# Kernel tuning notes

Measured on AMD Instinct MI355X. Metric: run time of the kernel, lower is better.

Reference implementation:

```python
import jax, jax.numpy as jnp
import numpy as np

# Reconstructed GTS forecasting module (DCGRU encoder-decoder, eval mode / no teacher forcing).
N = 5000        # nodes_num
U = 32          # rnn_units
IN = 1          # node_features per step
K = 2           # max_diffusion_step -> supports [X, A@X, A@A@X]
T_ENC = 12
T_DEC = 12
DIN = (K + 1) * (IN + U)


def setup_inputs() -> dict:
    key = jax.random.key(0)
    ks = jax.random.split(key, 12)
    def p(k, shape, scale=0.1):
        return jax.random.normal(k, shape, dtype=jnp.float32) * scale
    inputs = jax.random.normal(ks[0], (N, T_ENC), dtype=jnp.float32)
    targets = jax.random.normal(ks[1], (N, T_DEC), dtype=jnp.float32)
    adj = jax.random.uniform(ks[2], (N, N), dtype=jnp.float32)
    adj = adj / jnp.sum(adj, axis=1, keepdims=True)  # random-walk normalized support
    return {
        'inputs': inputs, 'targets': targets, 'adj_matrix': adj,
        'enc_Wg': p(ks[3], (DIN, 2 * U)), 'enc_bg': jnp.zeros((2 * U,), jnp.float32),
        'enc_Wc': p(ks[4], (DIN, U)),     'enc_bc': jnp.zeros((U,), jnp.float32),
        'dec_Wg': p(ks[5], (DIN, 2 * U)), 'dec_bg': jnp.zeros((2 * U,), jnp.float32),
        'dec_Wc': p(ks[6], (DIN, U)),     'dec_bc': jnp.zeros((U,), jnp.float32),
        'dec_Wp': p(ks[7], (U, 1)),       'dec_bp': jnp.zeros((1,), jnp.float32),
    }


def _gconv(x, h, adj, W, b):
    # diffusion graph convolution over supports [I, A, A^2]
    xh = jnp.concatenate([x, h], axis=-1)          # [N, IN+U]
    x1 = adj @ xh                                  # [N, IN+U]
    x2 = adj @ x1                                  # [N, IN+U]
    return jnp.concatenate([xh, x1, x2], axis=-1) @ W + b


def _dcgru_step(x, h, adj, Wg, bg, Wc, bc):
    ru = jax.nn.sigmoid(_gconv(x, h, adj, Wg, bg))  # [N, 2U]
    r, u = jnp.split(ru, 2, axis=-1)
    c = jnp.tanh(_gconv(x, r * h, adj, Wc, bc))
    return u * h + (1.0 - u) * c


def reference(inputs, targets, adj_matrix, enc_Wg, enc_bg, enc_Wc, enc_bc,
              dec_Wg, dec_bg, dec_Wc, dec_bc, dec_Wp, dec_bp):
    # ---- encoder: scan DCGRU over encoder_length timesteps ----
    def enc_step(h, xt):  # xt: [N]
        h = _dcgru_step(xt[:, None], h, adj_matrix, enc_Wg, enc_bg, enc_Wc, enc_bc)
        return h, None
    h0 = jnp.zeros((N, U), inputs.dtype)
    h_enc, _ = jax.lax.scan(enc_step, h0, inputs.T)
    go = jnp.zeros((N, 1), inputs.dtype)
    def dec_step(carry, _):
        h, x = carry
        h = _dcgru_step(x, h, adj_matrix, dec_Wg, dec_bg, dec_Wc, dec_bc)
        out = h @ dec_Wp + dec_bp  # [N, 1]
        return (h, out), out
    _, outs = jax.lax.scan(dec_step, (h_enc, go), None, length=T_DEC)
    # torch.cat(outputs, dim=-1) -> [N, T_DEC]
    return outs[:, :, 0].T
```

## Files before the change

### kernel.cpp

```cpp
#include <hip/hip_runtime.h>
#include <type_traits>

constexpr int NN = 5000;
constexpr int NP = 5120;
constexpr int TT = 12;
constexpr int UU = 32;
constexpr int FP = 48;
constexpr int FR = 33;
constexpr int DN = 99;
constexpr int BN = 16;
constexpr int BNODE = 32;
constexpr int KC = 128;
constexpr int NKC = NP / KC;
constexpr int CPW = NKC / 8;
constexpr int GRID_MM = (NN + BNODE - 1) / BNODE;
constexpr int CHE = FP * KC;
constexpr int ACH = BN * KC;
constexpr int PB = FP * BNODE;

typedef __attribute__((ext_vector_type(8))) short short8;
typedef __attribute__((ext_vector_type(4))) float f32x4;

__device__ __forceinline__ unsigned short f2bf(float x) {
  union { float f; unsigned u; } c; c.f = x;
  return (unsigned short)((c.u + 0x7FFFu + ((c.u >> 16) & 1u)) >> 16);
}

__device__ __forceinline__ int flatXF(int f, int node) {
  int chunk = node >> 7;
  int ks = (node >> 5) & 3;
  int q = (node >> 3) & 3;
  int j = node & 7;
  int t3 = f >> 4;
  int m = f & 15;
  return chunk * CHE + t3 * 2048 + ks * 512 + (m + 16 * q) * 8 + j;
}

__global__ void k_zero(uint4* __restrict__ p, int n) {
  int i = blockIdx.x * 256 + threadIdx.x;
  if (i < n) p[i] = make_uint4(0u, 0u, 0u, 0u);
}

__global__ void k_cast2(const float* __restrict__ adj, unsigned short* __restrict__ adjb) {
  int gid = blockIdx.x * 256 + threadIdx.x;
  int tile = gid >> 8;
  int r2 = gid & 255;
  int nt = tile / NKC, c = tile - nt * NKC;
  int ks = r2 >> 6;
  int qm = r2 & 63;
  int q = qm >> 4, m = qm & 15;
  int n = nt * 16 + m;
  int k = c * 128 + ks * 32 + q * 8;
  union { short8 s; unsigned short u[8]; } o;
  if (n < NN && k < NN) {
    const f32x4* a = reinterpret_cast<const f32x4*>(adj + (size_t)n * NN + k);
    f32x4 x0 = __builtin_nontemporal_load(a);
    f32x4 x1 = __builtin_nontemporal_load(a + 1);
    o.u[0] = f2bf(x0.x); o.u[1] = f2bf(x0.y); o.u[2] = f2bf(x0.z); o.u[3] = f2bf(x0.w);
    o.u[4] = f2bf(x1.x); o.u[5] = f2bf(x1.y); o.u[6] = f2bf(x1.z); o.u[7] = f2bf(x1.w);
  } else {
    o.u[0] = 0; o.u[1] = 0; o.u[2] = 0; o.u[3] = 0;
    o.u[4] = 0; o.u[5] = 0; o.u[6] = 0; o.u[7] = 0;
  }
  *reinterpret_cast<short8*>(adjb + (size_t)gid * 8) = o.s;
}

__global__ void k_initx0(const float* __restrict__ in, float* __restrict__ xf,
                         unsigned short* __restrict__ xb) {
  int n = blockIdx.x * 256 + threadIdx.x;
  if (n >= NP) return;
  float v = (n < NN) ? in[(size_t)n * TT] : 0.f;
  xf[n] = v;
  xb[flatXF(0, n)] = f2bf(v);
}

template <int EPI, bool USEBF>
__global__ __launch_bounds__(512, 2) void k_gemm(
    const unsigned short* __restrict__ adjb, const float* __restrict__ adjf,
    const unsigned short* __restrict__ rhs,
    float* __restrict__ outF, unsigned short* __restrict__ outB,
    const float* __restrict__ s0F, const float* __restrict__ s1F,
    const float* __restrict__ W, const float* __restrict__ bias,
    float* __restrict__ hT, float* __restrict__ uT,
    float* __restrict__ xoF, unsigned short* __restrict__ xoB,
    const float* __restrict__ inp, const float* __restrict__ Wp,
    const float* __restrict__ bp, float* __restrict__ dout,
    int mode, int tnext, int dstep) {
  constexpr int WC = (EPI == 1) ? 64 : 32;
  __shared__ float smemF[PB * 8 + FP * 33];
  float* Pv = smemF;
  float* x2s = smemF + PB * 8;
  float* Ws = smemF;

  const int tid = threadIdx.x;
  const int wave = tid >> 6;
  const int lane = tid & 63;
  const int m = lane & 15;
  const int q = lane >> 4;
  const int nodeBase = blockIdx.x * BNODE;

  f32x4 acc[2][3] = {};
  short8 aCur[2][4], aNxt[2][4];

  auto loadA = [&](int i, short8 (&b)[2][4]) {
    if constexpr (USEBF) {
      const int ch = wave * CPW + i;
#pragma unroll
      for (int h = 0; h < 2; ++h) {
        const unsigned short* a0 =
            adjb + ((size_t)(2 * blockIdx.x + h) * NKC + ch) * ACH + lane * 8;
#pragma unroll
        for (int ks = 0; ks < 4; ++ks)
          b[h][ks] = *reinterpret_cast<const short8*>(a0 + ks * 512);
      }
    } else {
      const int k0 = (wave * CPW + i) * KC;
#pragma unroll
      for (int h = 0; h < 2; ++h) {
        int gnh = nodeBase + h * 16 + m;
        const float* a0 = adjf + (size_t)((gnh < NN) ? gnh : NN - 1) * NN;
#pragma unroll
        for (int ks = 0; ks < 4; ++ks) {
          int kb = k0 + ks * 32 + q * 8;
          union { short8 s; unsigned short u[8]; } p0;
          if (kb + 8 <= NN) {
            float4 x0 = *(const float4*)(a0 + kb);
            float4 x1 = *(const float4*)(a0 + kb + 4);
            p0.u[0] = f2bf(x0.x); p0.u[1] = f2bf(x0.y); p0.u[2] = f2bf(x0.z); p0.u[3] = f2bf(x0.w);
            p0.u[4] = f2bf(x1.x); p0.u[5] = f2bf(x1.y); p0.u[6] = f2bf(x1.z); p0.u[7] = f2bf(x1.w);
          } else {
            for (int j = 0; j < 8; ++j) {
              int k = kb + j;
              p0.u[j] = (k < NN) ? f2bf(a0[k]) : (unsigned short)0;
            }
          }
          b[h][ks] = p0.s;
        }
      }
    }
  };

  loadA(0, aCur);
#pragma unroll
  for (int i = 0; i < CPW; ++i) {
    const int ch = wave * CPW + i;
    short8 cx[12];
    const unsigned short* xb = rhs + (size_t)ch * CHE + lane * 8;
#pragma unroll
    for (int t3 = 0; t3 < 3; ++t3)
#pragma unroll
      for (int ks = 0; ks < 4; ++ks)
        cx[t3 * 4 + ks] = *(const short8*)(xb + t3 * 2048 + ks * 512);
    if (i + 1 < CPW) loadA(i + 1, aNxt);
#pragma unroll
    for (int ks = 0; ks < 4; ++ks) {
#pragma unroll
      for (int h = 0; h < 2; ++h) {
        acc[h][0] = __builtin_amdgcn_mfma_f32_16x16x32_bf16(cx[ks], aCur[h][ks], acc[h][0], 0, 0, 0);
        acc[h][1] = __builtin_amdgcn_mfma_f32_16x16x32_bf16(cx[4 + ks], aCur[h][ks], acc[h][1], 0, 0, 0);
        acc[h][2] = __builtin_amdgcn_mfma_f32_16x16x32_bf16(cx[8 + ks], aCur[h][ks], acc[h][2], 0, 0, 0);
      }
    }
#pragma unroll
    for (int h = 0; h < 2; ++h)
#pragma unroll
      for (int ks = 0; ks < 4; ++ks) aCur[h][ks] = aNxt[h][ks];
  }

#pragma unroll
  for (int h = 0; h < 2; ++h)
#pragma unroll
    for (int t3 = 0; t3 < 3; ++t3)
#pragma unroll
      for (int r = 0; r < 4; ++r)
        Pv[wave * PB + (t3 * 16 + q * 4 + r) * BNODE + h * 16 + m] = acc[h][t3][r];
  __syncthreads();

  if constexpr (EPI == 0) {
    for (int e = tid; e < PB; e += 512) {
      int f = e >> 5, n = e & 31;
      float v = 0.f;
#pragma unroll
      for (int w = 0; w < 8; ++w) v += Pv[w * PB + e];
      int gn2 = nodeBase + n;
      if (gn2 >= NN) v = 0.f;
      outF[(size_t)f * NP + gn2] = v;
      outB[flatXF(f, gn2)] = f2bf(v);
    }
  } else {
    for (int e = tid; e < PB; e += 512) {
      int f = e >> 5, n = e & 31;
      float v = 0.f;
#pragma unroll
      for (int w = 0; w < 8; ++w) v += Pv[w * PB + e];
      x2s[f * 33 + n] = v;
    }
    __syncthreads();
    for (int i = tid; i < DN * WC; i += 512) Ws[i] = W[i];
    __syncthreads();
    const int nl = tid & 15;
    const int cg = tid >> 4;
    float hwv[2];
#pragma unroll
    for (int nh = 0; nh < 2; ++nh) {
      const int nl2 = nh * 16 + nl;
      const int gn2 = nodeBase + nl2;
      const bool valid = gn2 < NN;
      const int gnc = valid ? gn2 : NN - 1;
      if constexpr (EPI == 1) {
        float a0 = bias[cg], a1 = bias[cg + 32];
        for (int f = 0; f < FR; ++f) {
          float fe = s0F[(size_t)f * NP + gnc];
          a0 += fe * Ws[f * WC + cg]; a1 += fe * Ws[f * WC + cg + 32];
        }
        for (int f = 0; f < FR; ++f) {
          float fe = s1F[(size_t)f * NP + gnc];
          a0 += fe * Ws[(FR + f) * WC + cg]; a1 += fe * Ws[(FR + f) * WC + cg + 32];
        }
        for (int f = 0; f < FR; ++f) {
          float fe = x2s[f * 33 + nl2];
          a0 += fe * Ws[(2 * FR + f) * WC + cg]; a1 += fe * Ws[(2 * FR + f) * WC + cg + 32];
        }
        float r = 1.f / (1.f + expf(-a0));
        float hv = hT[(size_t)cg * NP + gnc];
        float xc = valid ? r * hv : 0.f;
        xoF[(size_t)(1 + cg) * NP + gn2] = xc;
        xoB[flatXF(1 + cg, gn2)] = f2bf(xc);
        float u = 1.f / (1.f + expf(-a1));
        uT[(size_t)cg * NP + gn2] = valid ? u : 0.f;
      } else {
        float a0 = bias[cg];
        for (int f = 0; f < FR; ++f) a0 += s0F[(size_t)f * NP + gnc] * Ws[f * WC + cg];
        for (int f = 0; f < FR; ++f) a0 += s1F[(size_t)f * NP + gnc] * Ws[(FR + f) * WC + cg];
        for (int f = 0; f < FR; ++f) a0 += x2s[f * 33 + nl2] * Ws[(2 * FR + f) * WC + cg];
        float c = tanhf(a0);
        float u = uT[(size_t)cg * NP + gnc];
        float h0 = hT[(size_t)cg * NP + gnc];
        float hn = u * h0 + (1.f - u) * c;
        float hw = valid ? hn : 0.f;
        hwv[nh] = hw;
        hT[(size_t)cg * NP + gn2] = hw;
        xoF[(size_t)(1 + cg) * NP + gn2] = hw;
        xoB[flatXF(1 + cg, gn2)] = f2bf(hw);
      }
    }
    if constexpr (EPI == 1) {
      if (tid < BNODE) {
        int g3 = nodeBase + tid;
        float v0 = s0F[g3];
        xoF[g3] = v0;
        xoB[flatXF(0, g3)] = f2bf(v0);
      }
    } else {
      __syncthreads();
      x2s[cg * 33 + nl] = hwv[0];
      x2s[cg * 33 + 16 + nl] = hwv[1];
      __syncthreads();
      if (tid < BNODE) {
        int g3 = nodeBase + tid;
        bool v3 = g3 < NN;
        float x0 = 0.f;
        if (mode == 0) {
          x0 = v3 ? inp[(size_t)g3 * TT + tnext] : 0.f;
        } else if (mode == 2) {
          float p = bp[0];
          for (int j = 0; j < UU; ++j) p += x2s[j * 33 + tid] * Wp[j];
          if (v3) dout[(size_t)g3 * TT + dstep] = p;
          x0 = v3 ? p : 0.f;
        }
        xoF[g3] = x0;
        xoB[flatXF(0, g3)] = f2bf(x0);
      }
    }
  }
}

extern "C" void kernel_launch(void* const* d_in, const int* in_sizes, int n_in,
                              void* d_out, int out_size, void* d_ws, size_t ws_size,
                              hipStream_t stream) {
  const float* inputs = (const float*)d_in[0];
  const float* adj = (const float*)d_in[2];
  const float* eWg = (const float*)d_in[3];
  const float* eBg = (const float*)d_in[4];
  const float* eWc = (const float*)d_in[5];
  const float* eBc = (const float*)d_in[6];
  const float* dWg = (const float*)d_in[7];
  const float* dBg = (const float*)d_in[8];
  const float* dWc = (const float*)d_in[9];
  const float* dBc = (const float*)d_in[10];
  const float* Wp = (const float*)d_in[11];
  const float* bp = (const float*)d_in[12];
  float* dout = (float*)d_out;

  char* ws = (char*)d_ws;
  size_t o = 0;
  float* xhGf = (float*)(ws + o); o += (size_t)FP * NP * 4;
  unsigned short* xhGb = (unsigned short*)(ws + o); o += (size_t)FP * NP * 2;
  float* xhCf = (float*)(ws + o); o += (size_t)FP * NP * 4;
  unsigned short* xhCb = (unsigned short*)(ws + o); o += (size_t)FP * NP * 2;
  float* x1f = (float*)(ws + o); o += (size_t)FP * NP * 4;
  unsigned short* x1b = (unsigned short*)(ws + o); o += (size_t)FP * NP * 2;
  float* hT = (float*)(ws + o); o += (size_t)UU * NP * 4;
  float* uT = (float*)(ws + o); o += (size_t)UU * NP * 4;
  size_t small = o;
  unsigned short* adjb = (unsigned short*)(ws + o);
  size_t need = o + (size_t)NP * NP * 2;
  bool usebf = ws_size >= need;

  k_zero<<<(int)((small / 16 + 255) / 256), 256, 0, stream>>>((uint4*)ws, (int)(small / 16));
  if (usebf) k_cast2<<<(NP / 8) * NP / 256, 256, 0, stream>>>(adj, adjb);
  k_initx0<<<NP / 256, 256, 0, stream>>>(inputs, xhGf, xhGb);

  auto run = [&](auto ubc) {
    constexpr bool UB = decltype(ubc)::value;
    const unsigned short* ab = UB ? adjb : nullptr;
    for (int t = 0; t < 2 * TT; ++t) {
      bool enc = t < TT;
      const float* Wg = enc ? eWg : dWg;
      const float* Bg = enc ? eBg : dBg;
      const float* Wc = enc ? eWc : dWc;
      const float* Bc = enc ? eBc : dBc;
      int mode, tn = 0, ds = 0;
      if (t < TT - 1) { mode = 0; tn = t + 1; }
      else if (t == TT - 1) { mode = 1; }
      else { mode = 2; ds = t - TT; }

      k_gemm<0, UB><<<GRID_MM, 512, 0, stream>>>(
          ab, adj, xhGb, x1f, x1b,
          nullptr, nullptr, nullptr, nullptr, nullptr, nullptr,
          nullptr, nullptr, nullptr, nullptr, nullptr, nullptr, 0, 0, 0);
      k_gemm<1, UB><<<GRID_MM, 512, 0, stream>>>(
          ab, adj, x1b, nullptr, nullptr,
          xhGf, x1f, Wg, Bg, hT, uT, xhCf, xhCb,
          nullptr, nullptr, nullptr, nullptr, 0, 0, 0);
      k_gemm<0, UB><<<GRID_MM, 512, 0, stream>>>(
          ab, adj, xhCb, x1f, x1b,
          nullptr, nullptr, nullptr, nullptr, nullptr, nullptr,
          nullptr, nullptr, nullptr, nullptr, nullptr, nullptr, 0, 0, 0);
      k_gemm<2, UB><<<GRID_MM, 512, 0, stream>>>(
          ab, adj, x1b, nullptr, nullptr,
          xhCf, x1f, Wc, Bc, hT, uT, xhGf, xhGb,
          inputs, Wp, bp, dout, mode, tn, ds);
    }
  };
  if (usebf) run(std::integral_constant<bool, true>{});
  else run(std::integral_constant<bool, false>{});
}
```

Measured before the change: 1.796 ms.

## Fuse all 96 per-step GEMM launches into one cooperative persistent kernel

Replaces the 96 separate kernel launches (four per timestep over 24 steps) with a single cooperative kernel. It loops over timesteps and separates the stages with grid.sync(), and extra __syncthreads() calls protect shared-memory reuse between stages. This removes per-launch overhead and the gaps between kernels. In exchange the grid must stay co-resident: 157 blocks of 512 threads at two blocks per CU. Grid barriers also add their own latency. The fp32 fallback path is kept as a separate kernel family.

```diff
diff --git a/kernel.cpp b/kernel.cpp
--- a/kernel.cpp
+++ b/kernel.cpp
@@ -1,5 +1,8 @@
 #include <hip/hip_runtime.h>
+#include <hip/hip_cooperative_groups.h>
 #include <type_traits>
+
+namespace cg = cooperative_groups;
 
 constexpr int NN = 5000;
 constexpr int NP = 5120;
@@ -74,9 +77,10 @@
   xb[flatXF(0, n)] = f2bf(v);
 }
 
-template <int EPI, bool USEBF>
-__global__ __launch_bounds__(512, 2) void k_gemm(
-    const unsigned short* __restrict__ adjb, const float* __restrict__ adjf,
+template <int EPI>
+__device__ __forceinline__ void gemm_stage(
+    float* __restrict__ smemF,
+    const unsigned short* __restrict__ adjb,
     const unsigned short* __restrict__ rhs,
     float* __restrict__ outF, unsigned short* __restrict__ outB,
     const float* __restrict__ s0F, const float* __restrict__ s1F,
@@ -87,7 +91,6 @@
     const float* __restrict__ bp, float* __restrict__ dout,
     int mode, int tnext, int dstep) {
   constexpr int WC = (EPI == 1) ? 64 : 32;
-  __shared__ float smemF[PB * 8 + FP * 33];
   float* Pv = smemF;
   float* x2s = smemF + PB * 8;
   float* Ws = smemF;
@@ -102,41 +105,19 @@
   f32x4 acc[2][3] = {};
   short8 aCur[2][4], aNxt[2][4];
 
+  const unsigned short* aB0 =
+      adjb + (size_t)(2 * blockIdx.x) * NKC * ACH + lane * 8;
+  const unsigned short* aB1 =
+      adjb + (size_t)(2 * blockIdx.x + 1) * NKC * ACH + lane * 8;
+
   auto loadA = [&](int i, short8 (&b)[2][4]) {
-    if constexpr (USEBF) {
-      const int ch = wave * CPW + i;
-#pragma unroll
-      for (int h = 0; h < 2; ++h) {
-        const unsigned short* a0 =
-            adjb + ((size_t)(2 * blockIdx.x + h) * NKC + ch) * ACH + lane * 8;
-#pragma unroll
-        for (int ks = 0; ks < 4; ++ks)
-          b[h][ks] = *reinterpret_cast<const short8*>(a0 + ks * 512);
-      }
-    } else {
-      const int k0 = (wave * CPW + i) * KC;
-#pragma unroll
-      for (int h = 0; h < 2; ++h) {
-        int gnh = nodeBase + h * 16 + m;
-        const float* a0 = adjf + (size_t)((gnh < NN) ? gnh : NN - 1) * NN;
-#pragma unroll
-        for (int ks = 0; ks < 4; ++ks) {
-          int kb = k0 + ks * 32 + q * 8;
-          union { short8 s; unsigned short u[8]; } p0;
-          if (kb + 8 <= NN) {
-            float4 x0 = *(const float4*)(a0 + kb);
-            float4 x1 = *(const float4*)(a0 + kb + 4);
-            p0.u[0] = f2bf(x0.x); p0.u[1] = f2bf(x0.y); p0.u[2] = f2bf(x0.z); p0.u[3] = f2bf(x0.w);
-            p0.u[4] = f2bf(x1.x); p0.u[5] = f2bf(x1.y); p0.u[6] = f2bf(x1.z); p0.u[7] = f2bf(x1.w);
-          } else {
-            for (int j = 0; j < 8; ++j) {
-              int k = kb + j;
-              p0.u[j] = (k < NN) ? f2bf(a0[k]) : (unsigned short)0;
-            }
-          }
-          b[h][ks] = p0.s;
-        }
-      }
+    const int ch = wave * CPW + i;
+    const unsigned short* a0 = aB0 + (size_t)ch * ACH;
+    const unsigned short* a1 = aB1 + (size_t)ch * ACH;
+#pragma unroll
+    for (int ks = 0; ks < 4; ++ks) {
+      b[0][ks] = *reinterpret_cast<const short8*>(a0 + ks * 512);
+      b[1][ks] = *reinterpret_cast<const short8*>(a1 + ks * 512);
     }
   };
 
@@ -187,6 +168,7 @@
       outF[(size_t)f * NP + gn2] = v;
       outB[flatXF(f, gn2)] = f2bf(v);
     }
+    __syncthreads();
   } else {
     for (int e = tid; e < PB; e += 512) {
       int f = e >> 5, n = e & 31;
@@ -228,6 +210,7 @@
         xoB[flatXF(1 + cg, gn2)] = f2bf(xc);
         float u = 1.f / (1.f + expf(-a1));
         uT[(size_t)cg * NP + gn2] = valid ? u : 0.f;
+        hwv[nh] = 0.f;
       } else {
         float a0 = bias[cg];
         for (int f = 0; f < FR; ++f) a0 += s0F[(size_t)f * NP + gnc] * Ws[f * WC + cg];
@@ -251,6 +234,7 @@
         xoF[g3] = v0;
         xoB[flatXF(0, g3)] = f2bf(v0);
       }
+      __syncthreads();
     } else {
       __syncthreads();
       x2s[cg * 33 + nl] = hwv[0];
@@ -271,6 +255,223 @@
         xoF[g3] = x0;
         xoB[flatXF(0, g3)] = f2bf(x0);
       }
+      __syncthreads();
+    }
+  }
+}
+
+struct MegaArgs {
+  const unsigned short* adjb;
+  unsigned short* xhGb; float* xhGf;
+  unsigned short* xhCb; float* xhCf;
+  unsigned short* x1b;  float* x1f;
+  float* hT; float* uT;
+  const float* eWg; const float* eBg; const float* eWc; const float* eBc;
+  const float* dWg; const float* dBg; const float* dWc; const float* dBc;
+  const float* Wp; const float* bp;
+  const float* inp; float* dout;
+};
+
+__global__ __launch_bounds__(512, 2) void k_mega(MegaArgs a) {
+  cg::grid_group grid = cg::this_grid();
+  __shared__ float smemF[PB * 8 + FP * 33];
+  for (int t = 0; t < 2 * TT; ++t) {
+    const bool enc = t < TT;
+    const float* Wg = enc ? a.eWg : a.dWg;
+    const float* Bg = enc ? a.eBg : a.dBg;
+    const float* Wc = enc ? a.eWc : a.dWc;
+    const float* Bc = enc ? a.eBc : a.dBc;
+    int mode, tn = 0, ds = 0;
+    if (t < TT - 1) { mode = 0; tn = t + 1; }
+    else if (t == TT - 1) { mode = 1; }
+    else { mode = 2; ds = t - TT; }
+
+    gemm_stage<0>(smemF, a.adjb, a.xhGb, a.x1f, a.x1b,
+                  nullptr, nullptr, nullptr, nullptr, nullptr, nullptr,
+                  nullptr, nullptr, nullptr, nullptr, nullptr, nullptr, 0, 0, 0);
+    grid.sync();
+    gemm_stage<1>(smemF, a.adjb, a.x1b, nullptr, nullptr,
+                  a.xhGf, a.x1f, Wg, Bg, a.hT, a.uT, a.xhCf, a.xhCb,
+                  nullptr, nullptr, nullptr, nullptr, 0, 0, 0);
+    grid.sync();
+    gemm_stage<0>(smemF, a.adjb, a.xhCb, a.x1f, a.x1b,
+                  nullptr, nullptr, nullptr, nullptr, nullptr, nullptr,
+                  nullptr, nullptr, nullptr, nullptr, nullptr, nullptr, 0, 0, 0);
+    grid.sync();
+    gemm_stage<2>(smemF, a.adjb, a.x1b, nullptr, nullptr,
+                  a.xhCf, a.x1f, Wc, Bc, a.hT, a.uT, a.xhGf, a.xhGb,
+                  a.inp, a.Wp, a.bp, a.dout, mode, tn, ds);
+    grid.sync();
+  }
+}
+
+template <int EPI>
+__global__ __launch_bounds__(512, 2) void k_gemm_f(
+    const float* __restrict__ adjf,
+    const unsigned short* __restrict__ rhs,
+    float* __restrict__ outF, unsigned short* __restrict__ outB,
+    const float* __restrict__ s0F, const float* __restrict__ s1F,
+    const float* __restrict__ W, const float* __restrict__ bias,
+    float* __restrict__ hT, float* __restrict__ uT,
+    float* __restrict__ xoF, unsigned short* __restrict__ xoB,
+    const float* __restrict__ inp, const float* __restrict__ Wp,
+    const float* __restrict__ bp, float* __restrict__ dout,
+    int mode, int tnext, int dstep) {
+  constexpr int WC = (EPI == 1) ? 64 : 32;
+  __shared__ float smemF[PB * 8 + FP * 33];
+  float* Pv = smemF;
+  float* x2s = smemF + PB * 8;
+  float* Ws = smemF;
+
+  const int tid = threadIdx.x;
+  const int wave = tid >> 6;
+  const int lane = tid & 63;
+  const int m = lane & 15;
+  const int q = lane >> 4;
+  const int nodeBase = blockIdx.x * BNODE;
+
+  f32x4 acc[2][3] = {};
+  for (int i = 0; i < CPW; ++i) {
+    const int ch = wave * CPW + i;
+    const int k0 = ch * KC;
+    short8 cx[12];
+    const unsigned short* xb = rhs + (size_t)ch * CHE + lane * 8;
+#pragma unroll
+    for (int t3 = 0; t3 < 3; ++t3)
+#pragma unroll
+      for (int ks = 0; ks < 4; ++ks)
+        cx[t3 * 4 + ks] = *(const short8*)(xb + t3 * 2048 + ks * 512);
+#pragma unroll
+    for (int h = 0; h < 2; ++h) {
+      int gnh = nodeBase + h * 16 + m;
+      const float* a0 = adjf + (size_t)((gnh < NN) ? gnh : NN - 1) * NN;
+#pragma unroll
+      for (int ks = 0; ks < 4; ++ks) {
+        int kb = k0 + ks * 32 + q * 8;
+        union { short8 s; unsigned short u[8]; } p0;
+        if (kb + 8 <= NN) {
+          float4 x0 = *(const float4*)(a0 + kb);
+          float4 x1 = *(const float4*)(a0 + kb + 4);
+          p0.u[0] = f2bf(x0.x); p0.u[1] = f2bf(x0.y); p0.u[2] = f2bf(x0.z); p0.u[3] = f2bf(x0.w);
+          p0.u[4] = f2bf(x1.x); p0.u[5] = f2bf(x1.y); p0.u[6] = f2bf(x1.z); p0.u[7] = f2bf(x1.w);
+        } else {
+          for (int j = 0; j < 8; ++j) {
+            int k = kb + j;
+            p0.u[j] = (k < NN) ? f2bf(a0[k]) : (unsigned short)0;
+          }
+        }
+        acc[h][0] = __builtin_amdgcn_mfma_f32_16x16x32_bf16(cx[ks], p0.s, acc[h][0], 0, 0, 0);
+        acc[h][1] = __builtin_amdgcn_mfma_f32_16x16x32_bf16(cx[4 + ks], p0.s, acc[h][1], 0, 0, 0);
+        acc[h][2] = __builtin_amdgcn_mfma_f32_16x16x32_bf16(cx[8 + ks], p0.s, acc[h][2], 0, 0, 0);
+      }
+    }
+  }
+
+#pragma unroll
+  for (int h = 0; h < 2; ++h)
+#pragma unroll
+    for (int t3 = 0; t3 < 3; ++t3)
+#pragma unroll
+      for (int r = 0; r < 4; ++r)
+        Pv[wave * PB + (t3 * 16 + q * 4 + r) * BNODE + h * 16 + m] = acc[h][t3][r];
+  __syncthreads();
+
+  if constexpr (EPI == 0) {
+    for (int e = tid; e < PB; e += 512) {
+      int f = e >> 5, n = e & 31;
+      float v = 0.f;
+#pragma unroll
+      for (int w = 0; w < 8; ++w) v += Pv[w * PB + e];
+      int gn2 = nodeBase + n;
+      if (gn2 >= NN) v = 0.f;
+      outF[(size_t)f * NP + gn2] = v;
+      outB[flatXF(f, gn2)] = f2bf(v);
+    }
+  } else {
+    for (int e = tid; e < PB; e += 512) {
+      int f = e >> 5, n = e & 31;
+      float v = 0.f;
+#pragma unroll
+      for (int w = 0; w < 8; ++w) v += Pv[w * PB + e];
+      x2s[f * 33 + n] = v;
+    }
+    __syncthreads();
+    for (int i = tid; i < DN * WC; i += 512) Ws[i] = W[i];
+    __syncthreads();
+    const int nl = tid & 15;
+    const int cg = tid >> 4;
+    float hwv[2];
+#pragma unroll
+    for (int nh = 0; nh < 2; ++nh) {
+      const int nl2 = nh * 16 + nl;
+      const int gn2 = nodeBase + nl2;
+      const bool valid = gn2 < NN;
+      const int gnc = valid ? gn2 : NN - 1;
+      if constexpr (EPI == 1) {
+        float a0 = bias[cg], a1 = bias[cg + 32];
+        for (int f = 0; f < FR; ++f) {
+          float fe = s0F[(size_t)f * NP + gnc];
+          a0 += fe * Ws[f * WC + cg]; a1 += fe * Ws[f * WC + cg + 32];
+        }
+        for (int f = 0; f < FR; ++f) {
+          float fe = s1F[(size_t)f * NP + gnc];
+          a0 += fe * Ws[(FR + f) * WC + cg]; a1 += fe * Ws[(FR + f) * WC + cg + 32];
+        }
+        for (int f = 0; f < FR; ++f) {
+          float fe = x2s[f * 33 + nl2];
+          a0 += fe * Ws[(2 * FR + f) * WC + cg]; a1 += fe * Ws[(2 * FR + f) * WC + cg + 32];
+        }
+        float r = 1.f / (1.f + expf(-a0));
+        float hv = hT[(size_t)cg * NP + gnc];
+        float xc = valid ? r * hv : 0.f;
+        xoF[(size_t)(1 + cg) * NP + gn2] = xc;
+        xoB[flatXF(1 + cg, gn2)] = f2bf(xc);
+        float u = 1.f / (1.f + expf(-a1));
+        uT[(size_t)cg * NP + gn2] = valid ? u : 0.f;
+        hwv[nh] = 0.f;
+      } else {
+        float a0 = bias[cg];
+        for (int f = 0; f < FR; ++f) a0 += s0F[(size_t)f * NP + gnc] * Ws[f * WC + cg];
+        for (int f = 0; f < FR; ++f) a0 += s1F[(size_t)f * NP + gnc] * Ws[(FR + f) * WC + cg];
+        for (int f = 0; f < FR; ++f) a0 += x2s[f * 33 + nl2] * Ws[(2 * FR + f) * WC + cg];
+        float c = tanhf(a0);
+        float u = uT[(size_t)cg * NP + gnc];
+        float h0 = hT[(size_t)cg * NP + gnc];
+        float hn = u * h0 + (1.f - u) * c;
+        float hw = valid ? hn : 0.f;
+        hwv[nh] = hw;
+        hT[(size_t)cg * NP + gn2] = hw;
+        xoF[(size_t)(1 + cg) * NP + gn2] = hw;
+        xoB[flatXF(1 + cg, gn2)] = f2bf(hw);
+      }
+    }
+    if constexpr (EPI == 1) {
+      if (tid < BNODE) {
+        int g3 = nodeBase + tid;
+        float v0 = s0F[g3];
+        xoF[g3] = v0;
+        xoB[flatXF(0, g3)] = f2bf(v0);
+      }
+    } else {
+      __syncthreads();
+      x2s[cg * 33 + nl] = hwv[0];
+      x2s[cg * 33 + 16 + nl] = hwv[1];
+      __syncthreads();
+      if (tid < BNODE) {
+        int g3 = nodeBase + tid;
+        bool v3 = g3 < NN;
+        float x0 = 0.f;
+        if (mode == 0) {
+          x0 = v3 ? inp[(size_t)g3 * TT + tnext] : 0.f;
+        } else if (mode == 2) {
+          float p = bp[0];
+          for (int j = 0; j < UU; ++j) p += x2s[j * 33 + tid] * Wp[j];
+          if (v3) dout[(size_t)g3 * TT + dstep] = p;
+          x0 = v3 ? p : 0.f;
+        }
+        xoF[g3] = x0;
+        xoB[flatXF(0, g3)] = f2bf(x0);
+      }
     }
   }
 }
@@ -311,9 +512,21 @@
   if (usebf) k_cast2<<<(NP / 8) * NP / 256, 256, 0, stream>>>(adj, adjb);
   k_initx0<<<NP / 256, 256, 0, stream>>>(inputs, xhGf, xhGb);
 
-  auto run = [&](auto ubc) {
-    constexpr bool UB = decltype(ubc)::value;
-    const unsigned short* ab = UB ? adjb : nullptr;
+  if (usebf) {
+    MegaArgs ha;
+    ha.adjb = adjb;
+    ha.xhGb = xhGb; ha.xhGf = xhGf;
+    ha.xhCb = xhCb; ha.xhCf = xhCf;
+    ha.x1b = x1b;   ha.x1f = x1f;
+    ha.hT = hT;     ha.uT = uT;
+    ha.eWg = eWg; ha.eBg = eBg; ha.eWc = eWc; ha.eBc = eBc;
+    ha.dWg = dWg; ha.dBg = dBg; ha.dWc = dWc; ha.dBc = dBc;
+    ha.Wp = Wp; ha.bp = bp;
+    ha.inp = inputs; ha.dout = dout;
+    void* kargs[] = {&ha};
+    hipLaunchCooperativeKernel((void*)k_mega, dim3(GRID_MM), dim3(512),
+                               kargs, 0, stream);
+  } else {
     for (int t = 0; t < 2 * TT; ++t) {
       bool enc = t < TT;
       const float* Wg = enc ? eWg : dWg;
@@ -325,24 +538,22 @@
       else if (t == TT - 1) { mode = 1; }
       else { mode = 2; ds = t - TT; }
 
-      k_gemm<0, UB><<<GRID_MM, 512, 0, stream>>>(
-          ab, adj, xhGb, x1f, x1b,
+      k_gemm_f<0><<<GRID_MM, 512, 0, stream>>>(
+          adj, xhGb, x1f, x1b,
           nullptr, nullptr, nullptr, nullptr, nullptr, nullptr,
           nullptr, nullptr, nullptr, nullptr, nullptr, nullptr, 0, 0, 0);
-      k_gemm<1, UB><<<GRID_MM, 512, 0, stream>>>(
-          ab, adj, x1b, nullptr, nullptr,
+      k_gemm_f<1><<<GRID_MM, 512, 0, stream>>>(
+          adj, x1b, nullptr, nullptr,
           xhGf, x1f, Wg, Bg, hT, uT, xhCf, xhCb,
           nullptr, nullptr, nullptr, nullptr, 0, 0, 0);
-      k_gemm<0, UB><<<GRID_MM, 512, 0, stream>>>(
-          ab, adj, xhCb, x1f, x1b,
+      k_gemm_f<0><<<GRID_MM, 512, 0, stream>>>(
+          adj, xhCb, x1f, x1b,
           nullptr, nullptr, nullptr, nullptr, nullptr, nullptr,
           nullptr, nullptr, nullptr, nullptr, nullptr, nullptr, 0, 0, 0);
-      k_gemm<2, UB><<<GRID_MM, 512, 0, stream>>>(
-          ab, adj, x1b, nullptr, nullptr,
+      k_gemm_f<2><<<GRID_MM, 512, 0, stream>>>(
+          adj, x1b, nullptr, nullptr,
           xhCf, x1f, Wc, Bc, hT, uT, xhGf, xhGb,
           inputs, Wp, bp, dout, mode, tn, ds);
     }
-  };
-  if (usebf) run(std::integral_constant<bool, true>{});
-  else run(std::integral_constant<bool, false>{});
-}
+  }
+}
```

Measured after the change: 6.451 ms. 259% more time.
